# Performance work log

Hardware: AMD Instinct MI355X
Metric: run time of the kernel (lower is better)

The kernel has to match this reference:

```python
import jax, jax.numpy as jnp
import numpy as np

T = 4          # number of atom types (H, C, N, O)
D = 384        # aev_length
H0, H1, H2 = 160, 128, 96
B, A = 2048, 64
ALPHA = 0.1    # CELU alpha


def celu(x, alpha=ALPHA):
    return jnp.where(x > 0, x, alpha * jnp.expm1(x / alpha))


def setup_inputs() -> dict:
    key = jax.random.key(0)
    ks = jax.random.split(key, 6)
    species = jax.random.randint(ks[0], (B, A), 0, T, dtype=jnp.int32)
    aev = jax.random.normal(ks[1], (B, A, D), dtype=jnp.float32)

    def w(k, shape, fan_in):
        return (jax.random.normal(k, shape, dtype=jnp.float32) / np.sqrt(fan_in)).astype(jnp.float32)

    # stacked per-type weights: leading axis T
    W0 = w(ks[2], (T, D, H0), D);   b0 = jnp.zeros((T, H0), jnp.float32)
    W1 = w(ks[3], (T, H0, H1), H0); b1 = jnp.zeros((T, H1), jnp.float32)
    W2 = w(ks[4], (T, H1, H2), H1); b2 = jnp.zeros((T, H2), jnp.float32)
    W3 = w(ks[5], (T, H2, 1), H2);  b3 = jnp.zeros((T, 1), jnp.float32)
    return dict(species=species, aev=aev,
                W0=W0, b0=b0, W1=W1, b1=b1, W2=W2, b2=b2, W3=W3, b3=b3)


def reference(species, aev, W0, b0, W1, b1, W2, b2, W3, b3):
    # species: [B, A] int32 in [0, T); aev: [B, A, D]
    sp = species.reshape(-1)            # [N]
    x = aev.reshape(-1, D)              # [N, D]
    # Run every type's MLP over all atoms (T is small), then select per atom.
    h = celu(jnp.einsum('nd,tdh->tnh', x, W0) + b0[:, None, :])   # [T, N, H0]
    h = celu(jnp.einsum('tnh,thk->tnk', h, W1) + b1[:, None, :])  # [T, N, H1]
    h = celu(jnp.einsum('tnk,tkm->tnm', h, W2) + b2[:, None, :])  # [T, N, H2]
    o = jnp.einsum('tnm,tmo->tno', h, W3) + b3[:, None, :]        # [T, N, 1]
    o = o[..., 0]                                                  # [T, N]
    per_atom = jnp.take_along_axis(o, sp[None, :], axis=0)[0]     # [N]
    energies = per_atom.reshape(species.shape).sum(axis=1)        # [B]
    return species, energies
```

## Files before the change

### kernel.cpp

```cpp
#include <hip/hip_runtime.h>
#include <hip/hip_bf16.h>

#define DD 384
#define NB 2048
#define NA 64
#define NN (NB*NA)

using bhalf8 = __attribute__((ext_vector_type(8))) __bf16;
using f32x4  = __attribute__((ext_vector_type(4))) float;
typedef unsigned short u16;
typedef unsigned char u8;

#define AS1 __attribute__((address_space(1)))
#define AS3 __attribute__((address_space(3)))

__device__ __forceinline__ void gl_lds16(const void* g, void* l) {
  __builtin_amdgcn_global_load_lds((const AS1 void*)g, (AS3 void*)l, 16, 0, 0);
}

__device__ __forceinline__ u16 f2b(float f) {
  __hip_bfloat16 h = __float2bfloat16(f);
  union { __hip_bfloat16 h; u16 u; } c; c.h = h; return c.u;
}
__device__ __forceinline__ float b2f(u16 u) {
  union { unsigned int i; float f; } c; c.i = ((unsigned int)u) << 16; return c.f;
}
__device__ __forceinline__ float celu_f(float v) {
  return v > 0.f ? v : 0.1f * (__expf(v * 10.f) - 1.f);
}
__device__ __forceinline__ bhalf8 pack8(float4 a, float4 b) {
  union { u16 us[8]; bhalf8 v; } t;
  t.us[0]=f2b(a.x); t.us[1]=f2b(a.y); t.us[2]=f2b(a.z); t.us[3]=f2b(a.w);
  t.us[4]=f2b(b.x); t.us[5]=f2b(b.y); t.us[6]=f2b(b.z); t.us[7]=f2b(b.w);
  return t.v;
}


__global__ void k_prep(const int* __restrict__ species, int* __restrict__ counts,
                       float* __restrict__ out_sp,
                       const float* __restrict__ W0, const float* __restrict__ W1,
                       const float* __restrict__ W2, const float* __restrict__ W3,
                       u16* __restrict__ W0img, u16* __restrict__ W1img,
                       u16* __restrict__ W2img, u16* __restrict__ W3B) {
  int tid = threadIdx.x;
  int id = blockIdx.x * 256 + tid;
  if (blockIdx.x < 512) {
    __shared__ int lcnt[4];
    if (tid < 4) lcnt[tid] = 0;
    __syncthreads();
    int s = species[id];
    out_sp[id] = (float)s;
    atomicAdd(&lcnt[s], 1);
    __syncthreads();
    if (tid < 4) atomicAdd(&counts[tid], lcnt[tid]);
  }
  if (id < 245760) {
    int t = id / 61440, r1 = id % 61440;
    int kc = r1 / 5120, r2 = r1 % 5120;
    int r = r2 >> 5, rem = r2 & 31, s = rem >> 3, e = rem & 7;
    int k = kc * 32 + (s ^ ((r >> 1) & 3)) * 8 + e;
    W0img[id] = f2b(W0[t * 61440 + k * 160 + r]);
  } else if ((id -= 245760) < 81920) {
    int t = id / 20480, r1 = id % 20480;
    int kc = r1 / 4096, r2 = r1 % 4096;
    int r = r2 >> 5, rem = r2 & 31, s = rem >> 3, e = rem & 7;
    int k = kc * 32 + (s ^ ((r >> 1) & 3)) * 8 + e;
    W1img[id] = f2b(W1[t * 20480 + k * 128 + r]);
  } else if ((id -= 81920) < 65536) {
    int t = id / 16384, r1 = id % 16384;
    int kc = r1 / 4096, r2 = r1 % 4096;
    int r = r2 >> 5, rem = r2 & 31, s = rem >> 3, e = rem & 7;
    u16 v = 0;
    if (r < 96) {
      int k = kc * 32 + (s ^ ((r >> 1) & 3)) * 8 + e;
      v = f2b(W2[t * 12288 + k * 96 + r]);
    }
    W2img[id] = v;
  } else if ((id -= 65536) < 384) {
    W3B[id] = f2b(W3[id]);
  }
}

__global__ void k_scatter(const int* __restrict__ species, const int* __restrict__ counts,
                          int* __restrict__ cursors, int* __restrict__ sorted) {
  __shared__ int lcnt[4];
  __shared__ int lbase[4];
  int tid = threadIdx.x;
  if (tid < 4) lcnt[tid] = 0;
  __syncthreads();
  int i = blockIdx.x * 256 + tid;
  int s = species[i];
  int lpos = atomicAdd(&lcnt[s], 1);
  __syncthreads();
  if (tid < 4) {
    int offs = 0;
    #pragma unroll
    for (int t = 0; t < 4; ++t) if (t < tid) offs += counts[t];
    lbase[tid] = offs + atomicAdd(&cursors[tid], lcnt[tid]);
  }
  __syncthreads();
  sorted[lbase[s] + lpos] = i;
}


__global__ __launch_bounds__(256, 5) void k_mlp(
    const float* __restrict__ aev, const int* __restrict__ sorted,
    const int* __restrict__ counts,
    const u16* __restrict__ W0img, const u16* __restrict__ W1img,
    const u16* __restrict__ W2img, const u16* __restrict__ W3B,
    const float* __restrict__ b0, const float* __restrict__ b1,
    const float* __restrict__ b2, const float* __restrict__ b3,
    float* __restrict__ atom_out)
{
  int type = blockIdx.x, tile = blockIdx.y;
  int c0 = counts[0], c1 = counts[1], c2 = counts[2], c3 = counts[3];
  int cnt = (type == 0) ? c0 : (type == 1) ? c1 : (type == 2) ? c2 : c3;
  if (tile * 64 >= cnt) return;
  int off = 0;
  if (type > 0) off += c0;
  if (type > 1) off += c1;
  if (type > 2) off += c2;

  __shared__ uint4 smem4[1344];
  u8* smem = (u8*)smem4;
  u8*  Ast = smem;
  u16* sH0 = (u16*)smem;
  u16* sH1 = (u16*)smem;
  u16* sH2 = (u16*)smem;

  int tid = threadIdx.x, lane = tid & 63, w = tid >> 6;
  int wm = w & 1, wn = w >> 1, l15 = lane & 15, lk = lane >> 4;
  int base = off + tile * 64, nvalid = min(64, cnt - tile * 64);

  int arow0 = w * 16 + (lane >> 3), arow1 = arow0 + 8;
  const float* a0 = aev + (size_t)sorted[base + min(arow0, nvalid - 1)] * DD
                    + (((lane & 7) ^ (arow0 & 7)) << 2);
  const float* a1 = aev + (size_t)sorted[base + min(arow1, nvalid - 1)] * DD
                    + (((lane & 7) ^ (arow1 & 7)) << 2);
  u8* dA = Ast + w * 2048;

#define STG_A(KC, B_) do { \
    gl_lds16(a0 + (KC) * 32, dA + (B_) * 8192); \
    gl_lds16(a1 + (KC) * 32, dA + (B_) * 8192 + 1024); \
  } while (0)

  int bsw = (lk ^ ((l15 >> 1) & 3)) << 4;
  const u8* gB0 = (const u8*)W0img + (size_t)type * 122880 + ((wn * 80 + l15) << 6) + bsw;
  int aoff0 = (wm * 32 + l15) * 128, aoff1 = aoff0 + 2048;
  int sAa = (((2 * lk)     ^ (l15 & 7)) << 4);
  int sAb = (((2 * lk + 1) ^ (l15 & 7)) << 4);

#define TOPW(WN) do { \
  asm volatile("s_waitcnt vmcnt(" #WN ")" ::: "memory"); \
  __builtin_amdgcn_sched_barrier(0); \
  __builtin_amdgcn_s_barrier(); \
  __builtin_amdgcn_sched_barrier(0); } while (0)
#define TAILW() do { \
  asm volatile("s_waitcnt lgkmcnt(0)" ::: "memory"); \
  __builtin_amdgcn_sched_barrier(0); \
  __builtin_amdgcn_s_barrier(); \
  __builtin_amdgcn_sched_barrier(0); } while (0)

  f32x4 acc0[2][5];
  #pragma unroll
  for (int mt = 0; mt < 2; ++mt)
    #pragma unroll
    for (int nt = 0; nt < 5; ++nt) acc0[mt][nt] = f32x4{0.f, 0.f, 0.f, 0.f};

  bhalf8 bf[5];
  STG_A(0, 0);
  #pragma unroll
  for (int nt = 0; nt < 5; ++nt) bf[nt] = *(const bhalf8*)(gB0 + nt * 1024);
  STG_A(1, 1);

#define PHA(KC, WN) \
  TOPW(WN); \
  { const u8* bA = Ast + ((KC) & 1) * 8192; \
    bhalf8 af0 = pack8(*(const float4*)(bA + aoff0 + sAa), *(const float4*)(bA + aoff0 + sAb)); \
    bhalf8 af1 = pack8(*(const float4*)(bA + aoff1 + sAa), *(const float4*)(bA + aoff1 + sAb)); \
    _Pragma("unroll") \
    for (int nt = 0; nt < 5; ++nt) { \
      acc0[0][nt] = __builtin_amdgcn_mfma_f32_16x16x32_bf16(af0, bf[nt], acc0[0][nt], 0, 0, 0); \
      acc0[1][nt] = __builtin_amdgcn_mfma_f32_16x16x32_bf16(af1, bf[nt], acc0[1][nt], 0, 0, 0); \
    } \
    if ((KC) < 11) { \
      _Pragma("unroll") \
      for (int nt = 0; nt < 5; ++nt) \
        bf[nt] = *(const bhalf8*)(gB0 + ((KC) + 1) * 10240 + nt * 1024); \
    } } \
  TAILW(); \
  if ((KC) < 10) STG_A((KC) + 2, (KC) & 1);

  PHA(0, 2)  PHA(1, 2)  PHA(2, 2)  PHA(3, 2)  PHA(4, 2)  PHA(5, 2)
  PHA(6, 2)  PHA(7, 2)  PHA(8, 2)  PHA(9, 2)  PHA(10, 2) PHA(11, 0)
#undef PHA
#undef STG_A

  #pragma unroll
  for (int mt = 0; mt < 2; ++mt)
    #pragma unroll
    for (int nt = 0; nt < 5; ++nt) {
      int col = wn * 80 + nt * 16 + l15;
      float bias = b0[type * 160 + col];
      #pragma unroll
      for (int i = 0; i < 4; ++i) {
        int row = wm * 32 + mt * 16 + lk * 4 + i;
        sH0[row * 168 + col] = f2b(celu_f(acc0[mt][nt][i] + bias));
      }
    }
  TAILW();

  const u8* gW1 = (const u8*)W1img + (size_t)type * 40960 + ((wn * 64 + l15) << 6) + bsw;
  f32x4 acc1[2][4];
  #pragma unroll
  for (int mt = 0; mt < 2; ++mt)
    #pragma unroll
    for (int nt = 0; nt < 4; ++nt) acc1[mt][nt] = f32x4{0.f, 0.f, 0.f, 0.f};

  #pragma unroll
  for (int kc = 0; kc < 5; ++kc) {
    bhalf8 af0 = *(const bhalf8*)&sH0[(wm * 32 + l15) * 168 + kc * 32 + lk * 8];
    bhalf8 af1 = *(const bhalf8*)&sH0[(wm * 32 + 16 + l15) * 168 + kc * 32 + lk * 8];
    bhalf8 bw[4];
    #pragma unroll
    for (int nt = 0; nt < 4; ++nt)
      bw[nt] = *(const bhalf8*)(gW1 + kc * 8192 + nt * 1024);
    #pragma unroll
    for (int nt = 0; nt < 4; ++nt) {
      acc1[0][nt] = __builtin_amdgcn_mfma_f32_16x16x32_bf16(af0, bw[nt], acc1[0][nt], 0, 0, 0);
      acc1[1][nt] = __builtin_amdgcn_mfma_f32_16x16x32_bf16(af1, bw[nt], acc1[1][nt], 0, 0, 0);
    }
  }
  TAILW();

  #pragma unroll
  for (int mt = 0; mt < 2; ++mt)
    #pragma unroll
    for (int nt = 0; nt < 4; ++nt) {
      int col = wn * 64 + nt * 16 + l15;
      float bias = b1[type * 128 + col];
      #pragma unroll
      for (int i = 0; i < 4; ++i) {
        int row = wm * 32 + mt * 16 + lk * 4 + i;
        sH1[row * 136 + col] = f2b(celu_f(acc1[mt][nt][i] + bias));
      }
    }
  TAILW();

  const u8* gW2 = (const u8*)W2img + (size_t)type * 32768 + ((wn * 48 + l15) << 6) + bsw;
  f32x4 acc2[2][3];
  #pragma unroll
  for (int mt = 0; mt < 2; ++mt)
    #pragma unroll
    for (int nt = 0; nt < 3; ++nt) acc2[mt][nt] = f32x4{0.f, 0.f, 0.f, 0.f};

  #pragma unroll
  for (int kc = 0; kc < 4; ++kc) {
    bhalf8 af0 = *(const bhalf8*)&sH1[(wm * 32 + l15) * 136 + kc * 32 + lk * 8];
    bhalf8 af1 = *(const bhalf8*)&sH1[(wm * 32 + 16 + l15) * 136 + kc * 32 + lk * 8];
    bhalf8 bw[3];
    #pragma unroll
    for (int nt = 0; nt < 3; ++nt)
      bw[nt] = *(const bhalf8*)(gW2 + kc * 8192 + nt * 1024);
    #pragma unroll
    for (int nt = 0; nt < 3; ++nt) {
      acc2[0][nt] = __builtin_amdgcn_mfma_f32_16x16x32_bf16(af0, bw[nt], acc2[0][nt], 0, 0, 0);
      acc2[1][nt] = __builtin_amdgcn_mfma_f32_16x16x32_bf16(af1, bw[nt], acc2[1][nt], 0, 0, 0);
    }
  }
  TAILW();

  #pragma unroll
  for (int mt = 0; mt < 2; ++mt)
    #pragma unroll
    for (int nt = 0; nt < 3; ++nt) {
      int col = wn * 48 + nt * 16 + l15;
      float bias = b2[type * 96 + col];
      #pragma unroll
      for (int i = 0; i < 4; ++i) {
        int row = wm * 32 + mt * 16 + lk * 4 + i;
        sH2[row * 104 + col] = f2b(celu_f(acc2[mt][nt][i] + bias));
      }
    }
  TAILW();

  {
    int atom = tid >> 2;
    int q = tid & 3;
    const u16* w3 = W3B + type * 96 + q * 24;
    const u16* hrow = sH2 + atom * 104 + q * 24;
    float s = 0.f;
    #pragma unroll
    for (int i = 0; i < 3; ++i) {
      union { bhalf8 v; u16 u[8]; } hu, wu2;
      hu.v = *(const bhalf8*)&hrow[i * 8];
      wu2.v = *(const bhalf8*)&w3[i * 8];
      #pragma unroll
      for (int j = 0; j < 8; ++j)
        s += b2f(hu.u[j]) * b2f(wu2.u[j]);
    }
    s += __shfl_xor(s, 1);
    s += __shfl_xor(s, 2);
    if (q == 0 && atom < nvalid)
      atom_out[sorted[base + atom]] = s + b3[type];
  }
}

__global__ void k_reduce(const float* __restrict__ atom_out, float* __restrict__ out_e) {
  int mol = blockIdx.x;
  int lane = threadIdx.x;
  float v = atom_out[mol * 64 + lane];
  #pragma unroll
  for (int m = 32; m >= 1; m >>= 1) v += __shfl_xor(v, m);
  if (lane == 0) out_e[mol] = v;
}


extern "C" void kernel_launch(void* const* d_in, const int* in_sizes, int n_in,
                              void* d_out, int out_size, void* d_ws, size_t ws_size,
                              hipStream_t stream) {
  const int*   species = (const int*)d_in[0];
  const float* aev = (const float*)d_in[1];
  const float* W0 = (const float*)d_in[2];
  const float* b0 = (const float*)d_in[3];
  const float* W1 = (const float*)d_in[4];
  const float* b1 = (const float*)d_in[5];
  const float* W2 = (const float*)d_in[6];
  const float* b2 = (const float*)d_in[7];
  const float* W3 = (const float*)d_in[8];
  const float* b3 = (const float*)d_in[9];
  float* out = (float*)d_out;

  unsigned char* ws = (unsigned char*)d_ws;
  int* counts = (int*)(ws + 0);
  int* sorted = (int*)(ws + 64);
  float* atom_out = (float*)(ws + 524352);
  u16* W0img = (u16*)(ws + 1048640);
  u16* W1img = (u16*)(ws + 1540160);
  u16* W2img = (u16*)(ws + 1704000);
  u16* W3B   = (u16*)(ws + 1835072);

  hipMemsetAsync(counts, 0, 48, stream);
  k_prep<<<1538, 256, 0, stream>>>(species, counts, out,
        W0, W1, W2, W3, W0img, W1img, W2img, W3B);
  k_scatter<<<NN / 256, 256, 0, stream>>>(species, counts, counts + 8, sorted);
  k_mlp<<<dim3(4, 2048), 256, 0, stream>>>(aev, sorted, counts,
        W0img, W1img, W2img, W3B, b0, b1, b2, b3, atom_out);
  k_reduce<<<NB, 64, 0, stream>>>(atom_out, out + NN);
}
```

Measured before the change: 80.17 us.

## Fuse species scatter into prep kernel and triple-buffer layer-0 A tiles

The separate scatter kernel is removed. Each species now scatters into its own fixed-size region (type*NN) inside the prep kernel, so no prior count pass or prefix offsets are needed and one launch disappears. The layer-0 A staging goes from double to triple buffering (LDS grows to 1536 uint4), which drops the per-step tail barrier in the K loop. This adds LDS use and a larger sorted workspace, and the barrier removal depends on TOPW still making async loads visible before they are read.

```diff
diff --git a/kernel.cpp b/kernel.cpp
--- a/kernel.cpp
+++ b/kernel.cpp
@@ -36,8 +36,8 @@
 }
 
 
-__global__ void k_prep(const int* __restrict__ species, int* __restrict__ counts,
-                       float* __restrict__ out_sp,
+__global__ void k_prep(const int* __restrict__ species, int* __restrict__ cursors,
+                       float* __restrict__ out_sp, int* __restrict__ sorted,
                        const float* __restrict__ W0, const float* __restrict__ W1,
                        const float* __restrict__ W2, const float* __restrict__ W3,
                        u16* __restrict__ W0img, u16* __restrict__ W1img,
@@ -46,13 +46,16 @@
   int id = blockIdx.x * 256 + tid;
   if (blockIdx.x < 512) {
     __shared__ int lcnt[4];
+    __shared__ int lbase[4];
     if (tid < 4) lcnt[tid] = 0;
     __syncthreads();
     int s = species[id];
     out_sp[id] = (float)s;
-    atomicAdd(&lcnt[s], 1);
+    int lpos = atomicAdd(&lcnt[s], 1);
     __syncthreads();
-    if (tid < 4) atomicAdd(&counts[tid], lcnt[tid]);
+    if (tid < 4) lbase[tid] = atomicAdd(&cursors[tid], lcnt[tid]);
+    __syncthreads();
+    sorted[s * NN + lbase[s] + lpos] = id;
   }
   if (id < 245760) {
     int t = id / 61440, r1 = id % 61440;
@@ -81,27 +84,6 @@
   }
 }
 
-__global__ void k_scatter(const int* __restrict__ species, const int* __restrict__ counts,
-                          int* __restrict__ cursors, int* __restrict__ sorted) {
-  __shared__ int lcnt[4];
-  __shared__ int lbase[4];
-  int tid = threadIdx.x;
-  if (tid < 4) lcnt[tid] = 0;
-  __syncthreads();
-  int i = blockIdx.x * 256 + tid;
-  int s = species[i];
-  int lpos = atomicAdd(&lcnt[s], 1);
-  __syncthreads();
-  if (tid < 4) {
-    int offs = 0;
-    #pragma unroll
-    for (int t = 0; t < 4; ++t) if (t < tid) offs += counts[t];
-    lbase[tid] = offs + atomicAdd(&cursors[tid], lcnt[tid]);
-  }
-  __syncthreads();
-  sorted[lbase[s] + lpos] = i;
-}
-
 
 __global__ __launch_bounds__(256, 5) void k_mlp(
     const float* __restrict__ aev, const int* __restrict__ sorted,
@@ -113,15 +95,10 @@
     float* __restrict__ atom_out)
 {
   int type = blockIdx.x, tile = blockIdx.y;
-  int c0 = counts[0], c1 = counts[1], c2 = counts[2], c3 = counts[3];
-  int cnt = (type == 0) ? c0 : (type == 1) ? c1 : (type == 2) ? c2 : c3;
+  int cnt = counts[type];
   if (tile * 64 >= cnt) return;
-  int off = 0;
-  if (type > 0) off += c0;
-  if (type > 1) off += c1;
-  if (type > 2) off += c2;
-
-  __shared__ uint4 smem4[1344];
+
+  __shared__ uint4 smem4[1536];
   u8* smem = (u8*)smem4;
   u8*  Ast = smem;
   u16* sH0 = (u16*)smem;
@@ -130,7 +107,7 @@
 
   int tid = threadIdx.x, lane = tid & 63, w = tid >> 6;
   int wm = w & 1, wn = w >> 1, l15 = lane & 15, lk = lane >> 4;
-  int base = off + tile * 64, nvalid = min(64, cnt - tile * 64);
+  int base = type * NN + tile * 64, nvalid = min(64, cnt - tile * 64);
 
   int arow0 = w * 16 + (lane >> 3), arow1 = arow0 + 8;
   const float* a0 = aev + (size_t)sorted[base + min(arow0, nvalid - 1)] * DD
@@ -175,7 +152,7 @@
 
 #define PHA(KC, WN) \
   TOPW(WN); \
-  { const u8* bA = Ast + ((KC) & 1) * 8192; \
+  { const u8* bA = Ast + ((KC) % 3) * 8192; \
     bhalf8 af0 = pack8(*(const float4*)(bA + aoff0 + sAa), *(const float4*)(bA + aoff0 + sAb)); \
     bhalf8 af1 = pack8(*(const float4*)(bA + aoff1 + sAa), *(const float4*)(bA + aoff1 + sAb)); \
     _Pragma("unroll") \
@@ -188,13 +165,14 @@
       for (int nt = 0; nt < 5; ++nt) \
         bf[nt] = *(const bhalf8*)(gB0 + ((KC) + 1) * 10240 + nt * 1024); \
     } } \
-  TAILW(); \
-  if ((KC) < 10) STG_A((KC) + 2, (KC) & 1);
+  if ((KC) < 10) STG_A((KC) + 2, ((KC) + 2) % 3);
 
   PHA(0, 2)  PHA(1, 2)  PHA(2, 2)  PHA(3, 2)  PHA(4, 2)  PHA(5, 2)
   PHA(6, 2)  PHA(7, 2)  PHA(8, 2)  PHA(9, 2)  PHA(10, 2) PHA(11, 0)
 #undef PHA
 #undef STG_A
+
+  TAILW();
 
   #pragma unroll
   for (int mt = 0; mt < 2; ++mt)
@@ -332,19 +310,18 @@
   float* out = (float*)d_out;
 
   unsigned char* ws = (unsigned char*)d_ws;
-  int* counts = (int*)(ws + 0);
+  int* cursors = (int*)(ws + 0);
   int* sorted = (int*)(ws + 64);
-  float* atom_out = (float*)(ws + 524352);
-  u16* W0img = (u16*)(ws + 1048640);
-  u16* W1img = (u16*)(ws + 1540160);
-  u16* W2img = (u16*)(ws + 1704000);
-  u16* W3B   = (u16*)(ws + 1835072);
-
-  hipMemsetAsync(counts, 0, 48, stream);
-  k_prep<<<1538, 256, 0, stream>>>(species, counts, out,
+  float* atom_out = (float*)(ws + 2097216);
+  u16* W0img = (u16*)(ws + 2621504);
+  u16* W1img = (u16*)(ws + 3113024);
+  u16* W2img = (u16*)(ws + 3276864);
+  u16* W3B   = (u16*)(ws + 3407936);
+
+  hipMemsetAsync(cursors, 0, 16, stream);
+  k_prep<<<1538, 256, 0, stream>>>(species, cursors, out, sorted,
         W0, W1, W2, W3, W0img, W1img, W2img, W3B);
-  k_scatter<<<NN / 256, 256, 0, stream>>>(species, counts, counts + 8, sorted);
-  k_mlp<<<dim3(4, 2048), 256, 0, stream>>>(aev, sorted, counts,
+  k_mlp<<<dim3(4, 2048), 256, 0, stream>>>(aev, sorted, cursors,
         W0img, W1img, W2img, W3B, b0, b1, b2, b3, atom_out);
   k_reduce<<<NB, 64, 0, stream>>>(atom_out, out + NN);
 }
```

Result: faster. 72.80 us (-9.2%).
